# Kernel tuning notes

Measured on AMD Instinct MI355X. Metric: run time of the kernel, lower is better.

The kernel has to match this reference:

```python
import math
import jax, jax.numpy as jnp
import numpy as np

B, T, T_P, C, H = 4, 2048, 256, 768, 12
HD = C // H


def setup_inputs() -> dict:
    key = jax.random.key(0)
    k1, k2, k3, k4 = jax.random.split(key, 4)
    x = jax.random.normal(k1, (B, T, C), dtype=jnp.float32)
    prefix = jax.random.normal(k2, (B, T_P, C), dtype=jnp.float32)
    # torch nn.Linear weight layout: (out_features, in_features)
    W_qkv = jax.random.normal(k3, (3 * C, C), dtype=jnp.float32) * (1.0 / math.sqrt(C))
    W_out = jax.random.normal(k4, (C, C), dtype=jnp.float32) * (1.0 / math.sqrt(C))
    return {"x": x, "prefix": prefix, "W_qkv": W_qkv, "W_out": W_out}


def _mac_causal_mask(t_p: int, t: int) -> jnp.ndarray:
    total = t_p + t
    mask = jnp.zeros((total, total), dtype=bool)
    mask = mask.at[:t_p, t_p:].set(True)  # h tokens blocked from x tokens
    causal = jnp.triu(jnp.ones((t, t), dtype=bool), k=1)  # causal within x block
    return mask.at[t_p:, t_p:].set(causal)


def reference(x, prefix, W_qkv, W_out):
    b, t, c = x.shape
    t_p = prefix.shape[1]
    t_all = t_p + t
    x_full = jnp.concatenate([prefix, x], axis=1)          # (B, T_all, C)
    qkv = x_full @ W_qkv.T                                  # (B, T_all, 3C)
    q, k, v = jnp.split(qkv, 3, axis=-1)
    # (B, H, T_all, HD)
    q = q.reshape(b, t_all, H, HD).transpose(0, 2, 1, 3)
    k = k.reshape(b, t_all, H, HD).transpose(0, 2, 1, 3)
    v = v.reshape(b, t_all, H, HD).transpose(0, 2, 1, 3)
    scale = 1.0 / math.sqrt(HD)
    att = jnp.einsum('bhqd,bhkd->bhqk', q, k) * scale       # (B, H, T_all, T_all)
    mask = _mac_causal_mask(t_p, t)
    att = jnp.where(mask[None, None], -jnp.inf, att)
    att = jax.nn.softmax(att, axis=-1)                      # dropout = identity (eval)
    out = jnp.einsum('bhqk,bhkd->bhqd', att, v)             # (B, H, T_all, HD)
    out = out.transpose(0, 2, 1, 3).reshape(b, t_all, c)
    out = out @ W_out.T
    return out[:, t_p:, :]                                  # only x portion (B, T, C)
```

## Files before the change

### kernel.cpp

```cpp
#include <hip/hip_runtime.h>

constexpr int Bn   = 4;
constexpr int Tn   = 2048;
constexpr int TPn  = 256;
constexpr int TALLn = 2304;
constexpr int Cn   = 768;
constexpr int Hn   = 12;
constexpr int HDn  = 64;

typedef __bf16 bf16x4 __attribute__((ext_vector_type(4)));
typedef __bf16 bf16x8 __attribute__((ext_vector_type(8)));
typedef float  f32x4  __attribute__((ext_vector_type(4)));
typedef unsigned u32x4 __attribute__((ext_vector_type(4)));

__device__ __forceinline__ unsigned short f2bf(float f) {
    unsigned int x = __float_as_uint(f);
    x += 0x7fffu + ((x >> 16) & 1u);
    return (unsigned short)(x >> 16);
}

__device__ __forceinline__ unsigned cvt_pk_bf16(float a, float b) {
    unsigned r;
    asm("v_cvt_pk_bf16_f32 %0, %1, %2" : "=v"(r) : "v"(a), "v"(b));
    return r;
}

#define ASYNC16(gsrc, ldst)                                                           \
    __builtin_amdgcn_global_load_lds((__attribute__((address_space(1))) void*)(gsrc), \
                                     (__attribute__((address_space(3))) void*)(ldst), \
                                     16, 0, 0)

__global__ __launch_bounds__(256) void k_build_xfull(
        const float* __restrict__ x, const float* __restrict__ pre,
        unsigned short* __restrict__ xf) {
    int idx = blockIdx.x * 256 + threadIdx.x;
    int row = idx / (Cn / 4);
    int c   = (idx - row * (Cn / 4)) * 4;
    int b = row / TALLn, tt = row - b * TALLn;
    const float* src = (tt < TPn) ? pre + ((size_t)b * TPn + tt) * Cn + c
                                  : x   + ((size_t)b * Tn + (tt - TPn)) * Cn + c;
    float4 f = *reinterpret_cast<const float4*>(src);
    ushort4 o = { f2bf(f.x), f2bf(f.y), f2bf(f.z), f2bf(f.w) };
    *reinterpret_cast<ushort4*>(xf + (size_t)row * Cn + c) = o;
}

__global__ __launch_bounds__(256) void k_cast(
        const float* __restrict__ in, unsigned short* __restrict__ out) {
    int idx = (blockIdx.x * 256 + threadIdx.x) * 4;
    float4 f = *reinterpret_cast<const float4*>(in + idx);
    ushort4 o = { f2bf(f.x), f2bf(f.y), f2bf(f.z), f2bf(f.w) };
    *reinterpret_cast<ushort4*>(out + idx) = o;
}

__global__ __launch_bounds__(256) void k_qkv_gemm(
        const unsigned short* __restrict__ A, const unsigned short* __restrict__ W,
        unsigned short* __restrict__ Qb, unsigned short* __restrict__ Kb,
        unsigned short* __restrict__ Vt) {
    __shared__ __align__(16) unsigned short smem[16384];
    unsigned short* As = smem;
    unsigned short* Bs = smem + 8192;
    const int tid  = threadIdx.x;
    const int wave = tid >> 6;
    const int lane = tid & 63;
    const int g = lane >> 4, l16 = lane & 15;
    const int m0 = blockIdx.x * 128, n0 = blockIdx.y * 128;
    const int wr = wave >> 1, wc = wave & 1;

    f32x4 acc[4][4] = {};

    for (int k0 = 0; k0 < Cn; k0 += 64) {
        #pragma unroll
        for (int inst = 0; inst < 4; ++inst) {
            const int li = inst * 256 + tid;
            const int row = li >> 3, slot = li & 7;
            const int ch = slot ^ (row & 7);
            ASYNC16(A + (size_t)(m0 + row) * Cn + k0 + ch * 8,
                    &As[(inst * 256 + wave * 64) * 8]);
            ASYNC16(W + (size_t)(n0 + row) * Cn + k0 + ch * 8,
                    &Bs[(inst * 256 + wave * 64) * 8]);
        }
        __syncthreads();
        #pragma unroll
        for (int kk = 0; kk < 2; ++kk) {
            bf16x8 af[4], bfv[4];
            #pragma unroll
            for (int mt = 0; mt < 4; ++mt) {
                const int row = wr * 64 + mt * 16 + l16;
                const int slot = (kk * 4 + g) ^ (row & 7);
                af[mt] = *reinterpret_cast<const bf16x8*>(&As[row * 64 + slot * 8]);
            }
            #pragma unroll
            for (int nt = 0; nt < 4; ++nt) {
                const int row = wc * 64 + nt * 16 + l16;
                const int slot = (kk * 4 + g) ^ (row & 7);
                bfv[nt] = *reinterpret_cast<const bf16x8*>(&Bs[row * 64 + slot * 8]);
            }
            #pragma unroll
            for (int mt = 0; mt < 4; ++mt)
                #pragma unroll
                for (int nt = 0; nt < 4; ++nt)
                    acc[mt][nt] = __builtin_amdgcn_mfma_f32_16x16x32_bf16(
                            af[mt], bfv[nt], acc[mt][nt], 0, 0, 0);
        }
        __syncthreads();
    }

    const int b   = m0 / TALLn;
    const int t0  = m0 - b * TALLn;
    const int sel = n0 / Cn;
    const int hn0 = n0 - sel * Cn;
    constexpr float SCQ = 0.18033688011112042f;

    if (sel == 2) {
        #pragma unroll
        for (int mt = 0; mt < 4; ++mt)
            #pragma unroll
            for (int nt = 0; nt < 4; ++nt)
                #pragma unroll
                for (int r = 0; r < 4; ++r) {
                    const int t  = wr * 64 + mt * 16 + g * 4 + r;
                    const int hn = wc * 64 + nt * 16 + l16;
                    smem[hn * 128 + (((t >> 3) ^ (hn & 7)) << 3) + (t & 7)] =
                            f2bf(acc[mt][nt][r]);
                }
        __syncthreads();
        #pragma unroll
        for (int j = 0; j < 8; ++j) {
            const int u  = tid + 256 * j;
            const int hn = u >> 4, tc = u & 15;
            const int tile64 = tc >> 3;
            const int np = tc & 7;
            const int kg = np >> 2, gs = np & 3;
            const int tgA = tile64 * 8 + kg * 4 + (gs >> 1);
            const int sub = (gs & 1) * 4;
            bf16x4 rA = *reinterpret_cast<const bf16x4*>(
                    &smem[hn * 128 + ((tgA ^ (hn & 7)) << 3) + sub]);
            bf16x4 rB = *reinterpret_cast<const bf16x4*>(
                    &smem[hn * 128 + (((tgA + 2) ^ (hn & 7)) << 3) + sub]);
            bf16x8 v = __builtin_shufflevector(rA, rB, 0, 1, 2, 3, 4, 5, 6, 7);
            const int hh = (hn0 + hn) >> 6;
            const int dd = hn & 63;
            *reinterpret_cast<bf16x8*>(
                    &Vt[(((size_t)b * Hn + hh) * HDn + dd) * TALLn + t0 + tc * 8]) = v;
        }
    } else {
        #pragma unroll
        for (int mt = 0; mt < 4; ++mt)
            #pragma unroll
            for (int nt = 0; nt < 4; ++nt)
                #pragma unroll
                for (int r = 0; r < 4; ++r) {
                    const int t  = t0 + wr * 64 + mt * 16 + g * 4 + r;
                    const int hn = hn0 + wc * 64 + nt * 16 + l16;
                    const int h = hn >> 6, d = hn & 63;
                    if (sel == 0)
                        Qb[(((size_t)b * Hn + h) * TALLn + t) * HDn + d] =
                                f2bf(acc[mt][nt][r] * SCQ);
                    else
                        Kb[(((size_t)b * Hn + h) * TALLn + t) * HDn + d] =
                                f2bf(acc[mt][nt][r]);
                }
    }
}

__global__ __launch_bounds__(256) void k_attn(
        const unsigned short* __restrict__ Qb, const unsigned short* __restrict__ Kb,
        const unsigned short* __restrict__ Vt, unsigned short* __restrict__ Ob) {
    __shared__ __align__(16) unsigned short Ks[2][4096];
    __shared__ __align__(16) unsigned short Vs[2][4096];
    const int tid  = threadIdx.x;
    const int wq   = tid >> 6;
    const int lane = tid & 63;
    const int l16  = lane & 15;
    const int g    = lane >> 4;

    const int fb  = blockIdx.x;
    const int j   = fb >> 3;
    const int bh  = 6 * (fb & 7) + (j % 6);
    const int chunk = 31 - (j / 6);
    const int nkt = 5 + chunk;
    const size_t kv = (size_t)bh * TALLn * HDn;

    int koff[4][2];
    #pragma unroll
    for (int band = 0; band < 4; ++band)
        #pragma unroll
        for (int ks = 0; ks < 2; ++ks)
            koff[band][ks] = (band * 16 + l16) * 64 + (((ks * 4 + g) ^ (l16 & 7)) << 3);
    int voff[2];
    #pragma unroll
    for (int kg = 0; kg < 2; ++kg)
        voff[kg] = l16 * 64 + (((kg * 4 + g) ^ (l16 & 7)) << 3);
    const unsigned short* pk[2];
    const unsigned short* pv[2];
    int sdst[2];
    #pragma unroll
    for (int inst = 0; inst < 2; ++inst) {
        const int li = inst * 256 + tid;
        const int row = li >> 3;
        const int ch = (li & 7) ^ (row & 7);
        pk[inst] = Kb + kv + row * HDn + ch * 8;
        pv[inst] = Vt + kv + row * TALLn + ch * 8;
        sdst[inst] = (inst * 256 + wq * 64) * 8;
    }
    constexpr int KSTRIDE = 64 * HDn;
    constexpr int VSTRIDE = 64;

    bf16x8 qf[2];
    {
        const int tq = TPn + chunk * 64 + wq * 16 + l16;
        #pragma unroll
        for (int ks = 0; ks < 2; ++ks)
            qf[ks] = *reinterpret_cast<const bf16x8*>(
                    Qb + kv + (size_t)tq * HDn + ks * 32 + g * 8);
    }

    bf16x8 ones;
    #pragma unroll
    for (int i = 0; i < 8; ++i) ones[i] = (__bf16)1.0f;

    f32x4 oacc[4] = {};
    f32x4 lacc = {};

    #pragma unroll
    for (int inst = 0; inst < 2; ++inst) {
        ASYNC16(pk[inst], &Ks[0][0] + sdst[inst]);
        ASYNC16(pv[inst], &Vs[0][0] + sdst[inst]);
        pk[inst] += KSTRIDE;
        pv[inst] += VSTRIDE;
    }
    __syncthreads();

    int buf = 0;
    for (int t = 0; t < nkt; ++t) {
        if (t + 1 < nkt) {
            #pragma unroll
            for (int inst = 0; inst < 2; ++inst) {
                ASYNC16(pk[inst], &Ks[buf ^ 1][0] + sdst[inst]);
                ASYNC16(pv[inst], &Vs[buf ^ 1][0] + sdst[inst]);
                pk[inst] += KSTRIDE;
                pv[inst] += VSTRIDE;
            }
        }
        const unsigned short* Ksb = &Ks[buf][0];
        const unsigned short* Vsb = &Vs[buf][0];

        f32x4 sacc[4] = {};
        __builtin_amdgcn_s_setprio(1);
        #pragma unroll
        for (int band = 0; band < 4; ++band) {
            bf16x8 k0 = *reinterpret_cast<const bf16x8*>(&Ksb[koff[band][0]]);
            bf16x8 k1 = *reinterpret_cast<const bf16x8*>(&Ksb[koff[band][1]]);
            sacc[band] = __builtin_amdgcn_mfma_f32_16x16x32_bf16(
                    k0, qf[0], sacc[band], 0, 0, 0);
            sacc[band] = __builtin_amdgcn_mfma_f32_16x16x32_bf16(
                    k1, qf[1], sacc[band], 0, 0, 0);
        }
        __builtin_amdgcn_s_setprio(0);

        if (t == nkt - 1) {
            const int lim = TPn + chunk * 64 + wq * 16 + l16 - t * 64;
            #pragma unroll
            for (int band = 0; band < 4; ++band)
                #pragma unroll
                for (int r = 0; r < 4; ++r)
                    sacc[band][r] = (band * 16 + g * 4 + r <= lim) ? sacc[band][r]
                                                                   : -1e30f;
        }
        unsigned dwb[4][2];
        #pragma unroll
        for (int band = 0; band < 4; ++band) {
            const float e0 = exp2f(sacc[band][0]);
            const float e1 = exp2f(sacc[band][1]);
            const float e2 = exp2f(sacc[band][2]);
            const float e3 = exp2f(sacc[band][3]);
            dwb[band][0] = cvt_pk_bf16(e0, e1);
            dwb[band][1] = cvt_pk_bf16(e2, e3);
        }

        __builtin_amdgcn_s_setprio(1);
        #pragma unroll
        for (int kg = 0; kg < 2; ++kg) {
            const u32x4 uu = { dwb[2 * kg][0], dwb[2 * kg][1],
                               dwb[2 * kg + 1][0], dwb[2 * kg + 1][1] };
            const bf16x8 pf = __builtin_bit_cast(bf16x8, uu);
            lacc = __builtin_amdgcn_mfma_f32_16x16x32_bf16(ones, pf, lacc, 0, 0, 0);
            #pragma unroll
            for (int dband = 0; dband < 4; ++dband) {
                bf16x8 vf = *reinterpret_cast<const bf16x8*>(
                        &Vsb[dband * 1024 + voff[kg]]);
                oacc[dband] = __builtin_amdgcn_mfma_f32_16x16x32_bf16(
                        vf, pf, oacc[dband], 0, 0, 0);
            }
        }
        __builtin_amdgcn_s_setprio(0);

        buf ^= 1;
        __syncthreads();
    }

    const int b = bh / Hn, h = bh - b * Hn;
    const float inv = 1.0f / lacc[0];
    const size_t row = (size_t)b * Tn + chunk * 64 + wq * 16 + l16;
    #pragma unroll
    for (int dband = 0; dband < 4; ++dband) {
        ushort4 st;
        st.x = f2bf(oacc[dband][0] * inv);
        st.y = f2bf(oacc[dband][1] * inv);
        st.z = f2bf(oacc[dband][2] * inv);
        st.w = f2bf(oacc[dband][3] * inv);
        *reinterpret_cast<ushort4*>(&Ob[row * Cn + h * 64 + dband * 16 + g * 4]) = st;
    }
}

__global__ __launch_bounds__(256) void k_out_gemm(
        const unsigned short* __restrict__ A, const unsigned short* __restrict__ W,
        float* __restrict__ out) {
    __shared__ __align__(16) unsigned short As[8192];
    __shared__ __align__(16) unsigned short Bs[8192];
    const int tid  = threadIdx.x;
    const int wave = tid >> 6;
    const int lane = tid & 63;
    const int g = lane >> 4, l16 = lane & 15;
    const int m0 = blockIdx.x * 128, n0 = blockIdx.y * 128;
    const int wr = wave >> 1, wc = wave & 1;

    f32x4 acc[4][4] = {};

    for (int k0 = 0; k0 < Cn; k0 += 64) {
        #pragma unroll
        for (int inst = 0; inst < 4; ++inst) {
            const int li = inst * 256 + tid;
            const int row = li >> 3, slot = li & 7;
            const int ch = slot ^ (row & 7);
            ASYNC16(A + (size_t)(m0 + row) * Cn + k0 + ch * 8,
                    &As[(inst * 256 + wave * 64) * 8]);
            ASYNC16(W + (size_t)(n0 + row) * Cn + k0 + ch * 8,
                    &Bs[(inst * 256 + wave * 64) * 8]);
        }
        __syncthreads();
        #pragma unroll
        for (int kk = 0; kk < 2; ++kk) {
            bf16x8 af[4], bfv[4];
            #pragma unroll
            for (int mt = 0; mt < 4; ++mt) {
                const int row = wr * 64 + mt * 16 + l16;
                const int slot = (kk * 4 + g) ^ (row & 7);
                af[mt] = *reinterpret_cast<const bf16x8*>(&As[row * 64 + slot * 8]);
            }
            #pragma unroll
            for (int nt = 0; nt < 4; ++nt) {
                const int row = wc * 64 + nt * 16 + l16;
                const int slot = (kk * 4 + g) ^ (row & 7);
                bfv[nt] = *reinterpret_cast<const bf16x8*>(&Bs[row * 64 + slot * 8]);
            }
            #pragma unroll
            for (int mt = 0; mt < 4; ++mt)
                #pragma unroll
                for (int nt = 0; nt < 4; ++nt)
                    acc[mt][nt] = __builtin_amdgcn_mfma_f32_16x16x32_bf16(
                            af[mt], bfv[nt], acc[mt][nt], 0, 0, 0);
        }
        __syncthreads();
    }

    #pragma unroll
    for (int mt = 0; mt < 4; ++mt)
        #pragma unroll
        for (int nt = 0; nt < 4; ++nt)
            #pragma unroll
            for (int r = 0; r < 4; ++r) {
                const int m = m0 + wr * 64 + mt * 16 + g * 4 + r;
                const int n = n0 + wc * 64 + nt * 16 + l16;
                out[(size_t)m * Cn + n] = acc[mt][nt][r];
            }
}

extern "C" void kernel_launch(void* const* d_in, const int* in_sizes, int n_in,
                              void* d_out, int out_size, void* d_ws, size_t ws_size,
                              hipStream_t stream) {
    const float* x    = (const float*)d_in[0];
    const float* pre  = (const float*)d_in[1];
    const float* wqkv = (const float*)d_in[2];
    const float* wout = (const float*)d_in[3];
    float* out = (float*)d_out;
    char* ws = (char*)d_ws;

    unsigned short* xf  = (unsigned short*)(ws + 0);
    unsigned short* wqb = (unsigned short*)(ws + 14155776);
    unsigned short* wob = (unsigned short*)(ws + 17694720);
    unsigned short* Qb  = (unsigned short*)(ws + 18874368);
    unsigned short* Kb  = (unsigned short*)(ws + 33030144);
    unsigned short* Vt  = (unsigned short*)(ws + 47185920);
    unsigned short* Ob  = (unsigned short*)(ws + 61341696);

    k_build_xfull<<<dim3((Bn * TALLn * Cn / 4) / 256), 256, 0, stream>>>(x, pre, xf);
    k_cast<<<dim3((3 * Cn * Cn / 4) / 256), 256, 0, stream>>>(wqkv, wqb);
    k_cast<<<dim3((Cn * Cn / 4) / 256), 256, 0, stream>>>(wout, wob);
    k_qkv_gemm<<<dim3((Bn * TALLn) / 128, (3 * Cn) / 128), 256, 0, stream>>>(
            xf, wqb, Qb, Kb, Vt);
    k_attn<<<dim3(1536), 256, 0, stream>>>(Qb, Kb, Vt, Ob);
    k_out_gemm<<<dim3((Bn * Tn) / 128, Cn / 128), 256, 0, stream>>>(Ob, wob, out);
}
```

Measured before the change: 143.0 us.

## Double-buffer LDS in projection GEMMs with BK=32 and merge weight casts

```diff
diff --git a/kernel.cpp b/kernel.cpp
--- a/kernel.cpp
+++ b/kernel.cpp
@@ -44,12 +44,18 @@
     *reinterpret_cast<ushort4*>(xf + (size_t)row * Cn + c) = o;
 }
 
-__global__ __launch_bounds__(256) void k_cast(
-        const float* __restrict__ in, unsigned short* __restrict__ out) {
+__global__ __launch_bounds__(256) void k_cast2(
+        const float* __restrict__ wqkv, const float* __restrict__ wout,
+        unsigned short* __restrict__ wqb, unsigned short* __restrict__ wob) {
     int idx = (blockIdx.x * 256 + threadIdx.x) * 4;
-    float4 f = *reinterpret_cast<const float4*>(in + idx);
+    const int n1 = 3 * Cn * Cn;
+    const float* src;
+    unsigned short* dst;
+    if (idx < n1) { src = wqkv + idx; dst = wqb + idx; }
+    else          { src = wout + (idx - n1); dst = wob + (idx - n1); }
+    float4 f = *reinterpret_cast<const float4*>(src);
     ushort4 o = { f2bf(f.x), f2bf(f.y), f2bf(f.z), f2bf(f.w) };
-    *reinterpret_cast<ushort4*>(out + idx) = o;
+    *reinterpret_cast<ushort4*>(dst) = o;
 }
 
 __global__ __launch_bounds__(256) void k_qkv_gemm(
@@ -57,8 +63,6 @@
         unsigned short* __restrict__ Qb, unsigned short* __restrict__ Kb,
         unsigned short* __restrict__ Vt) {
     __shared__ __align__(16) unsigned short smem[16384];
-    unsigned short* As = smem;
-    unsigned short* Bs = smem + 8192;
     const int tid  = threadIdx.x;
     const int wave = tid >> 6;
     const int lane = tid & 63;
@@ -66,42 +70,66 @@
     const int m0 = blockIdx.x * 128, n0 = blockIdx.y * 128;
     const int wr = wave >> 1, wc = wave & 1;
 
+    const unsigned short* pa[2];
+    const unsigned short* pb[2];
+    int sd[2];
+    #pragma unroll
+    for (int inst = 0; inst < 2; ++inst) {
+        const int li = inst * 256 + tid;
+        const int row = li >> 2;
+        const int ch = (li & 3) ^ ((row >> 1) & 3);
+        pa[inst] = A + (size_t)(m0 + row) * Cn + ch * 8;
+        pb[inst] = W + (size_t)(n0 + row) * Cn + ch * 8;
+        sd[inst] = (inst * 256 + wave * 64) * 8;
+    }
+    int aoff[4], boff[4];
+    #pragma unroll
+    for (int mt = 0; mt < 4; ++mt) {
+        const int ra = wr * 64 + mt * 16 + l16;
+        aoff[mt] = ra * 32 + ((g ^ ((ra >> 1) & 3)) << 3);
+        const int rb = wc * 64 + mt * 16 + l16;
+        boff[mt] = rb * 32 + ((g ^ ((rb >> 1) & 3)) << 3);
+    }
+
     f32x4 acc[4][4] = {};
 
-    for (int k0 = 0; k0 < Cn; k0 += 64) {
-        #pragma unroll
-        for (int inst = 0; inst < 4; ++inst) {
-            const int li = inst * 256 + tid;
-            const int row = li >> 3, slot = li & 7;
-            const int ch = slot ^ (row & 7);
-            ASYNC16(A + (size_t)(m0 + row) * Cn + k0 + ch * 8,
-                    &As[(inst * 256 + wave * 64) * 8]);
-            ASYNC16(W + (size_t)(n0 + row) * Cn + k0 + ch * 8,
-                    &Bs[(inst * 256 + wave * 64) * 8]);
-        }
-        __syncthreads();
-        #pragma unroll
-        for (int kk = 0; kk < 2; ++kk) {
-            bf16x8 af[4], bfv[4];
-            #pragma unroll
-            for (int mt = 0; mt < 4; ++mt) {
-                const int row = wr * 64 + mt * 16 + l16;
-                const int slot = (kk * 4 + g) ^ (row & 7);
-                af[mt] = *reinterpret_cast<const bf16x8*>(&As[row * 64 + slot * 8]);
+    #pragma unroll
+    for (int inst = 0; inst < 2; ++inst) {
+        ASYNC16(pa[inst], &smem[0]    + sd[inst]);
+        ASYNC16(pb[inst], &smem[8192] + sd[inst]);
+        pa[inst] += 32;
+        pb[inst] += 32;
+    }
+    __syncthreads();
+
+    int buf = 0;
+    for (int kk = 0; kk < 24; ++kk) {
+        if (kk + 1 < 24) {
+            #pragma unroll
+            for (int inst = 0; inst < 2; ++inst) {
+                ASYNC16(pa[inst], &smem[(buf ^ 1) * 4096]        + sd[inst]);
+                ASYNC16(pb[inst], &smem[8192 + (buf ^ 1) * 4096] + sd[inst]);
+                pa[inst] += 32;
+                pb[inst] += 32;
             }
-            #pragma unroll
-            for (int nt = 0; nt < 4; ++nt) {
-                const int row = wc * 64 + nt * 16 + l16;
-                const int slot = (kk * 4 + g) ^ (row & 7);
-                bfv[nt] = *reinterpret_cast<const bf16x8*>(&Bs[row * 64 + slot * 8]);
-            }
-            #pragma unroll
-            for (int mt = 0; mt < 4; ++mt)
-                #pragma unroll
-                for (int nt = 0; nt < 4; ++nt)
-                    acc[mt][nt] = __builtin_amdgcn_mfma_f32_16x16x32_bf16(
-                            af[mt], bfv[nt], acc[mt][nt], 0, 0, 0);
-        }
+        }
+        const unsigned short* Ab = &smem[buf * 4096];
+        const unsigned short* Bb = &smem[8192 + buf * 4096];
+        bf16x8 af[4], bfv[4];
+        #pragma unroll
+        for (int mt = 0; mt < 4; ++mt) {
+            af[mt]  = *reinterpret_cast<const bf16x8*>(&Ab[aoff[mt]]);
+            bfv[mt] = *reinterpret_cast<const bf16x8*>(&Bb[boff[mt]]);
+        }
+        __builtin_amdgcn_s_setprio(1);
+        #pragma unroll
+        for (int mt = 0; mt < 4; ++mt)
+            #pragma unroll
+            for (int nt = 0; nt < 4; ++nt)
+                acc[mt][nt] = __builtin_amdgcn_mfma_f32_16x16x32_bf16(
+                        af[mt], bfv[nt], acc[mt][nt], 0, 0, 0);
+        __builtin_amdgcn_s_setprio(0);
+        buf ^= 1;
         __syncthreads();
     }
 
@@ -316,8 +344,7 @@
 __global__ __launch_bounds__(256) void k_out_gemm(
         const unsigned short* __restrict__ A, const unsigned short* __restrict__ W,
         float* __restrict__ out) {
-    __shared__ __align__(16) unsigned short As[8192];
-    __shared__ __align__(16) unsigned short Bs[8192];
+    __shared__ __align__(16) unsigned short smem[16384];
     const int tid  = threadIdx.x;
     const int wave = tid >> 6;
     const int lane = tid & 63;
@@ -325,42 +352,66 @@
     const int m0 = blockIdx.x * 128, n0 = blockIdx.y * 128;
     const int wr = wave >> 1, wc = wave & 1;
 
+    const unsigned short* pa[2];
+    const unsigned short* pb[2];
+    int sd[2];
+    #pragma unroll
+    for (int inst = 0; inst < 2; ++inst) {
+        const int li = inst * 256 + tid;
+        const int row = li >> 2;
+        const int ch = (li & 3) ^ ((row >> 1) & 3);
+        pa[inst] = A + (size_t)(m0 + row) * Cn + ch * 8;
+        pb[inst] = W + (size_t)(n0 + row) * Cn + ch * 8;
+        sd[inst] = (inst * 256 + wave * 64) * 8;
+    }
+    int aoff[4], boff[4];
+    #pragma unroll
+    for (int mt = 0; mt < 4; ++mt) {
+        const int ra = wr * 64 + mt * 16 + l16;
+        aoff[mt] = ra * 32 + ((g ^ ((ra >> 1) & 3)) << 3);
+        const int rb = wc * 64 + mt * 16 + l16;
+        boff[mt] = rb * 32 + ((g ^ ((rb >> 1) & 3)) << 3);
+    }
+
     f32x4 acc[4][4] = {};
 
-    for (int k0 = 0; k0 < Cn; k0 += 64) {
-        #pragma unroll
-        for (int inst = 0; inst < 4; ++inst) {
-            const int li = inst * 256 + tid;
-            const int row = li >> 3, slot = li & 7;
-            const int ch = slot ^ (row & 7);
-            ASYNC16(A + (size_t)(m0 + row) * Cn + k0 + ch * 8,
-                    &As[(inst * 256 + wave * 64) * 8]);
-            ASYNC16(W + (size_t)(n0 + row) * Cn + k0 + ch * 8,
-                    &Bs[(inst * 256 + wave * 64) * 8]);
-        }
-        __syncthreads();
-        #pragma unroll
-        for (int kk = 0; kk < 2; ++kk) {
-            bf16x8 af[4], bfv[4];
-            #pragma unroll
-            for (int mt = 0; mt < 4; ++mt) {
-                const int row = wr * 64 + mt * 16 + l16;
-                const int slot = (kk * 4 + g) ^ (row & 7);
-                af[mt] = *reinterpret_cast<const bf16x8*>(&As[row * 64 + slot * 8]);
+    #pragma unroll
+    for (int inst = 0; inst < 2; ++inst) {
+        ASYNC16(pa[inst], &smem[0]    + sd[inst]);
+        ASYNC16(pb[inst], &smem[8192] + sd[inst]);
+        pa[inst] += 32;
+        pb[inst] += 32;
+    }
+    __syncthreads();
+
+    int buf = 0;
+    for (int kk = 0; kk < 24; ++kk) {
+        if (kk + 1 < 24) {
+            #pragma unroll
+            for (int inst = 0; inst < 2; ++inst) {
+                ASYNC16(pa[inst], &smem[(buf ^ 1) * 4096]        + sd[inst]);
+                ASYNC16(pb[inst], &smem[8192 + (buf ^ 1) * 4096] + sd[inst]);
+                pa[inst] += 32;
+                pb[inst] += 32;
             }
-            #pragma unroll
-            for (int nt = 0; nt < 4; ++nt) {
-                const int row = wc * 64 + nt * 16 + l16;
-                const int slot = (kk * 4 + g) ^ (row & 7);
-                bfv[nt] = *reinterpret_cast<const bf16x8*>(&Bs[row * 64 + slot * 8]);
-            }
-            #pragma unroll
-            for (int mt = 0; mt < 4; ++mt)
-                #pragma unroll
-                for (int nt = 0; nt < 4; ++nt)
-                    acc[mt][nt] = __builtin_amdgcn_mfma_f32_16x16x32_bf16(
-                            af[mt], bfv[nt], acc[mt][nt], 0, 0, 0);
-        }
+        }
+        const unsigned short* Ab = &smem[buf * 4096];
+        const unsigned short* Bb = &smem[8192 + buf * 4096];
+        bf16x8 af[4], bfv[4];
+        #pragma unroll
+        for (int mt = 0; mt < 4; ++mt) {
+            af[mt]  = *reinterpret_cast<const bf16x8*>(&Ab[aoff[mt]]);
+            bfv[mt] = *reinterpret_cast<const bf16x8*>(&Bb[boff[mt]]);
+        }
+        __builtin_amdgcn_s_setprio(1);
+        #pragma unroll
+        for (int mt = 0; mt < 4; ++mt)
+            #pragma unroll
+            for (int nt = 0; nt < 4; ++nt)
+                acc[mt][nt] = __builtin_amdgcn_mfma_f32_16x16x32_bf16(
+                        af[mt], bfv[nt], acc[mt][nt], 0, 0, 0);
+        __builtin_amdgcn_s_setprio(0);
+        buf ^= 1;
         __syncthreads();
     }
 
@@ -395,8 +446,7 @@
     unsigned short* Ob  = (unsigned short*)(ws + 61341696);
 
     k_build_xfull<<<dim3((Bn * TALLn * Cn / 4) / 256), 256, 0, stream>>>(x, pre, xf);
-    k_cast<<<dim3((3 * Cn * Cn / 4) / 256), 256, 0, stream>>>(wqkv, wqb);
-    k_cast<<<dim3((Cn * Cn / 4) / 256), 256, 0, stream>>>(wout, wob);
+    k_cast2<<<dim3((4 * Cn * Cn / 4) / 256), 256, 0, stream>>>(wqkv, wout, wqb, wob);
     k_qkv_gemm<<<dim3((Bn * TALLn) / 128, (3 * Cn) / 128), 256, 0, stream>>>(
             xf, wqb, Qb, Kb, Vt);
     k_attn<<<dim3(1536), 256, 0, stream>>>(Qb, Kb, Vt, Ob);
```

After: 141.2 us. No clear change (-1.3%).
